# Kernel optimization log

Hardware: AMD Instinct MI355X
Metric: run time of the kernel (lower is better)

Reference implementation:

```python
import jax, jax.numpy as jnp
import numpy as np

WINDOW = 2


def _fo_pool(h, f):
    """c_t = f_t * c_{t-1} + (1 - f_t) * h_t with c_{-1} = 0, scanned over axis 1 (time).
    Implemented as an associative scan on affine maps (a, b): c -> a*c + b."""
    def combine(left, right):
        a1, b1 = left
        a2, b2 = right
        return a2 * a1, a2 * b1 + b2
    a = f
    b = (1.0 - f) * h
    _, c = jax.lax.associative_scan(combine, (a, b), axis=1)
    return c


def setup_inputs() -> dict:
    key = jax.random.key(0)
    k1, k2 = jax.random.split(key)
    B, T, C, U = 8, 2048, 1024, 1024
    x = jax.random.normal(k1, (B, T, C), dtype=jnp.float32)
    # Keras Conv1D kernel layout: [window, in_channels, out_channels]; glorot-ish scale
    scale = (2.0 / (C + 3 * U)) ** 0.5
    kernel = jax.random.normal(k2, (WINDOW, C, 3 * U), dtype=jnp.float32) * scale
    bias = jnp.zeros((3 * U,), dtype=jnp.float32)
    return {"x": x, "kernel": kernel, "bias": bias}


def reference(x, kernel, bias):
    # causal conv1d: pad (window-1) on the left of time axis
    gv = jax.lax.conv_general_dilated(
        x, kernel,
        window_strides=(1,),
        padding=[(WINDOW - 1, 0)],
        dimension_numbers=("NWC", "WIO", "NWC"),
    ) + bias  # [B, T, 3U]
    hidden, forget, output = jnp.split(gv, 3, axis=-1)
    hidden = jnp.tanh(hidden)
    forget = jax.nn.sigmoid(forget)
    c = _fo_pool(hidden, forget)           # [B, T, U]
    h = jax.nn.sigmoid(output) * c          # output gate
    return h
```

## Files before the change

### kernel.cpp

```cpp
#include <hip/hip_runtime.h>


typedef _Float16 f16;
typedef _Float16 f16x8 __attribute__((ext_vector_type(8)));
typedef float    f32x4 __attribute__((ext_vector_type(4)));

#define Bq 8
#define Tq 2048
#define Cq 1024
#define Uq 1024
#define Mq (Bq*Tq)
#define Kq (2*Cq)
#define Nq (3*Uq)
#define NCH 32
#define CHL (Tq/NCH)

#define AS1 __attribute__((address_space(1)))
#define AS3 __attribute__((address_space(3)))

__global__ void prep_xs(const float* __restrict__ x, f16* __restrict__ Xs) {
    long long idx = ((long long)blockIdx.x * blockDim.x + threadIdx.x) * 8;
    int c = (int)(idx & (Cq - 1));
    long long row = idx >> 10;
    int tp = (int)(row % (Tq + 1));
    int b  = (int)(row / (Tq + 1));
    f16x8 o;
    if (tp == 0) {
#pragma unroll
        for (int j = 0; j < 8; j++) o[j] = (f16)0.0f;
    } else {
        const float* src = x + (((size_t)b * Tq + (tp - 1)) << 10) + c;
        float4 v0 = *(const float4*)(src);
        float4 v1 = *(const float4*)(src + 4);
        o[0]=(f16)v0.x; o[1]=(f16)v0.y; o[2]=(f16)v0.z; o[3]=(f16)v0.w;
        o[4]=(f16)v1.x; o[5]=(f16)v1.y; o[6]=(f16)v1.z; o[7]=(f16)v1.w;
    }
    *(f16x8*)(Xs + idx) = o;
}

__global__ void prep_wt(const float* __restrict__ w, f16* __restrict__ WT) {
    __shared__ float t[32][33];
    int kb = blockIdx.x * 32, nb = blockIdx.y * 32;
    int tx = threadIdx.x & 31, ty = threadIdx.x >> 5;
#pragma unroll
    for (int j = 0; j < 32; j += 8)
        t[ty + j][tx] = w[(size_t)(kb + ty + j) * Nq + nb + tx];
    __syncthreads();
#pragma unroll
    for (int j = 0; j < 32; j += 8)
        WT[(size_t)(nb + ty + j) * Kq + kb + tx] = (f16)t[tx][ty + j];
}

__global__ __launch_bounds__(512, 2) void gemm_gates8(
    const f16* __restrict__ Xs, const f16* __restrict__ WT,
    const float* __restrict__ bias,
    f16* __restrict__ H, f16* __restrict__ F, f16* __restrict__ O)
{
    __shared__ __align__(16) f16 smem[65536];
    const int tid  = threadIdx.x;
    const int lane = tid & 63;
    const int wave = tid >> 6;
    const int wm = wave >> 2;
    const int wn = wave & 3;

    const int wg  = blockIdx.x;
    const int swz = (wg & 7) * 96 + (wg >> 3);
    const int mT  = swz / 12, nT = swz - mT * 12;
    const int rM  = mT * 256;
    const int nB  = nT * 256;
    const int b   = rM >> 11;
    const int t0  = rM & (Tq - 1);
    const size_t xsRow0 = (size_t)b * (Tq + 1) + t0;

    const int srow = tid >> 3;
    const int scol = (((tid & 7) ^ (srow & 7))) * 8;
    const f16* Abase = Xs + (xsRow0 + srow) * (size_t)Cq + scol;
    const f16* Bbase = WT + (size_t)(nB + srow) * Kq + scol;
    const int dstT = tid * 16;

#define STAGE_A(c, h, kt) do { \
    const f16* _s = Abase + (size_t)((h) * 128) * Cq + (kt) * 64; \
    int _d = (c) * 65536 + (h) * 16384 + dstT; \
    __builtin_amdgcn_global_load_lds((const AS1 void*)_s, \
        (AS3 void*)((char*)smem + _d), 16, 0, 0); \
    __builtin_amdgcn_global_load_lds((const AS1 void*)(_s + (size_t)64 * Cq), \
        (AS3 void*)((char*)smem + _d + 8192), 16, 0, 0); \
} while (0)

#define STAGE_B(c, h, kt) do { \
    const f16* _s = Bbase + (size_t)((h) * 128) * Kq + (kt) * 64; \
    int _d = 32768 + (c) * 65536 + (h) * 16384 + dstT; \
    __builtin_amdgcn_global_load_lds((const AS1 void*)_s, \
        (AS3 void*)((char*)smem + _d), 16, 0, 0); \
    __builtin_amdgcn_global_load_lds((const AS1 void*)(_s + (size_t)64 * Kq), \
        (AS3 void*)((char*)smem + _d + 8192), 16, 0, 0); \
} while (0)

    const int rAoff = (wm * 64 + (lane & 15)) * 128;
    const int rBoff = (wn * 32 + (lane & 15)) * 128;
    const int ksw0 = (((lane >> 4) * 16)) ^ ((lane & 7) << 4);
    const int ksw1 = (64 + ((lane >> 4) * 16)) ^ ((lane & 7) << 4);

    f32x4 acc[2][2][4][2] = {};
    f16x8 af[4][2], bg0[2][2], bg1[2][2];

#define LOADA(c, h) do { \
    const char* _a = (const char*)smem + (c) * 65536 + (h) * 16384 + rAoff; \
    _Pragma("unroll") \
    for (int mi = 0; mi < 4; mi++) { \
        af[mi][0] = *(const f16x8*)(_a + mi * 2048 + ksw0); \
        af[mi][1] = *(const f16x8*)(_a + mi * 2048 + ksw1); \
    } \
} while (0)

#define LOADB(c, g, breg) do { \
    const char* _b = (const char*)smem + 32768 + (c) * 65536 + (g) * 16384 + rBoff; \
    _Pragma("unroll") \
    for (int ni = 0; ni < 2; ni++) { \
        breg[ni][0] = *(const f16x8*)(_b + ni * 2048 + ksw0); \
        breg[ni][1] = *(const f16x8*)(_b + ni * 2048 + ksw1); \
    } \
} while (0)

#define MM(h, g, breg) do { \
    _Pragma("unroll") \
    for (int mi = 0; mi < 4; mi++) \
    _Pragma("unroll") \
    for (int ni = 0; ni < 2; ni++) { \
        acc[h][g][mi][ni] = __builtin_amdgcn_mfma_f32_16x16x32_f16(af[mi][0], breg[ni][0], acc[h][g][mi][ni], 0, 0, 0); \
        acc[h][g][mi][ni] = __builtin_amdgcn_mfma_f32_16x16x32_f16(af[mi][1], breg[ni][1], acc[h][g][mi][ni], 0, 0, 0); \
    } \
} while (0)

#define BAR() __builtin_amdgcn_s_barrier()
#define LGKM0() do { asm volatile("s_waitcnt lgkmcnt(0)" ::: "memory"); \
                     __builtin_amdgcn_sched_barrier(0); } while (0)
#define VM4() asm volatile("s_waitcnt vmcnt(4)" ::: "memory")

#define KTILE(c, ktn) do { \
     LOADA(c, 0); LOADB(c, 0, bg0); STAGE_A(1 - (c), 0, ktn); BAR(); LGKM0(); \
           __builtin_amdgcn_s_setprio(1); MM(0, 0, bg0); __builtin_amdgcn_s_setprio(0); VM4(); BAR(); \
     LOADB(c, 1, bg1); STAGE_B(1 - (c), 0, ktn); BAR(); LGKM0(); \
           __builtin_amdgcn_s_setprio(1); MM(0, 1, bg1); __builtin_amdgcn_s_setprio(0); VM4(); BAR(); \
     LOADA(c, 1); STAGE_B(1 - (c), 1, ktn); BAR(); LGKM0(); \
           __builtin_amdgcn_s_setprio(1); MM(1, 0, bg0); __builtin_amdgcn_s_setprio(0); BAR(); \
     STAGE_A(1 - (c), 1, ktn); BAR(); LGKM0(); \
           __builtin_amdgcn_s_setprio(1); MM(1, 1, bg1); __builtin_amdgcn_s_setprio(0); VM4(); BAR(); \
} while (0)

    STAGE_A(0, 0, 0); STAGE_B(0, 0, 0); STAGE_B(0, 1, 0); STAGE_A(0, 1, 0);
    asm volatile("s_waitcnt vmcnt(4)" ::: "memory");
    BAR();

    for (int t = 0; t < 32; t += 2) {
        KTILE(0, t + 1);
        KTILE(1, t + 2);
    }

    const int gate = nB >> 10;
    f16* G = (gate == 0) ? H : ((gate == 1) ? F : O);
#pragma unroll
    for (int h = 0; h < 2; h++)
#pragma unroll
    for (int g = 0; g < 2; g++)
#pragma unroll
    for (int ni = 0; ni < 2; ni++) {
        const int col = nB + g * 128 + wn * 32 + ni * 16 + (lane & 15);
        const int u = col & (Uq - 1);
        const float bv = bias[col];
#pragma unroll
        for (int mi = 0; mi < 4; mi++)
#pragma unroll
        for (int j = 0; j < 4; j++) {
            const int row = rM + h * 128 + wm * 64 + mi * 16 + ((lane >> 4) << 2) + j;
            float v = acc[h][g][mi][ni][j] + bv;
            float r;
            if (gate == 0) r = 1.0f - 2.0f / (__expf(2.0f * v) + 1.0f);
            else           r = 1.0f / (1.0f + __expf(-v));
            G[(size_t)row * Uq + u] = (f16)r;
        }
    }
}

__global__ void scan_pass1(const f16* __restrict__ F, const f16* __restrict__ H,
                           float* __restrict__ Ach, float* __restrict__ Bch) {
    int idx = blockIdx.x * blockDim.x + threadIdx.x;
    int u  = idx & (Uq - 1);
    int ch = (idx >> 10) & (NCH - 1);
    int b  = idx >> 15;
    size_t base = ((size_t)b * Tq + ch * CHL) * Uq + u;
    float a = 1.0f, c = 0.0f;
    for (int i = 0; i < CHL; i++) {
        float f = (float)F[base + (size_t)i * Uq];
        float h = (float)H[base + (size_t)i * Uq];
        c = f * c + (1.0f - f) * h;
        a *= f;
    }
    Ach[idx] = a;
    Bch[idx] = c;
}

__global__ void scan_pass2(const float* __restrict__ Ach, const float* __restrict__ Bch,
                           float* __restrict__ Cin) {
    int idx = blockIdx.x * blockDim.x + threadIdx.x;
    int u = idx & (Uq - 1);
    int b = idx >> 10;
    float c = 0.0f;
    for (int ch = 0; ch < NCH; ch++) {
        int o = ((b * NCH) + ch) * Uq + u;
        Cin[o] = c;
        c = Ach[o] * c + Bch[o];
    }
}

__global__ void scan_pass3(const f16* __restrict__ F, const f16* __restrict__ H,
                           const f16* __restrict__ O, const float* __restrict__ Cin,
                           float* __restrict__ out) {
    int idx = blockIdx.x * blockDim.x + threadIdx.x;
    int u  = idx & (Uq - 1);
    int ch = (idx >> 10) & (NCH - 1);
    int b  = idx >> 15;
    size_t base = ((size_t)b * Tq + ch * CHL) * Uq + u;
    float c = Cin[idx];
    for (int i = 0; i < CHL; i++) {
        float f = (float)F[base + (size_t)i * Uq];
        float h = (float)H[base + (size_t)i * Uq];
        c = f * c + (1.0f - f) * h;
        out[base + (size_t)i * Uq] = (float)O[base + (size_t)i * Uq] * c;
    }
}

extern "C" void kernel_launch(void* const* d_in, const int* in_sizes, int n_in,
                              void* d_out, int out_size, void* d_ws, size_t ws_size,
                              hipStream_t stream) {
    const float* x    = (const float*)d_in[0];
    const float* w    = (const float*)d_in[1];
    const float* bias = (const float*)d_in[2];
    float* out = (float*)d_out;
    char* ws = (char*)d_ws;

    f16* Xs   = (f16*)(ws);
    f16* WT   = (f16*)(ws + 33570816);
    f16* Hh   = (f16*)(ws + 46153728);
    f16* Fh   = (f16*)(ws + 79708160);
    f16* Oh   = (f16*)(ws + 113262592);
    float* Ach = (float*)(ws + 146817024);
    float* Bch = (float*)(ws + 147865600);
    float* Cin = (float*)(ws + 148914176);

    prep_xs<<<(Bq * (Tq + 1) * Cq) / (8 * 256), 256, 0, stream>>>(x, Xs);
    prep_wt<<<dim3(Kq / 32, Nq / 32), 256, 0, stream>>>(w, WT);
    gemm_gates8<<<(Mq / 256) * (Nq / 256), 512, 0, stream>>>(Xs, WT, bias, Hh, Fh, Oh);
    scan_pass1<<<(Bq * NCH * Uq) / 256, 256, 0, stream>>>(Fh, Hh, Ach, Bch);
    scan_pass2<<<(Bq * Uq) / 256, 256, 0, stream>>>(Ach, Bch, Cin);
    scan_pass3<<<(Bq * NCH * Uq) / 256, 256, 0, stream>>>(Fh, Hh, Oh, Cin, out);
}
```

Measured before the change: 261.8 us.

## Double-buffer A fragments and overlap LDS reads with MFMA using partial waitcnts

Splits the A register fragments into two buffers so the next fragment loads from LDS can be issued while MFMAs on the current fragments run. Full lgkmcnt(0) waits are replaced with partial lgkmcnt counts, several barriers are removed, and vmcnt waits are tightened from 4 to 2. The next tile's first A/B fragments are preloaded at the end of each k-tile. This raises register pressure and makes correctness depend on the chosen waitcnt counts and barrier placement.

```diff
diff --git a/kernel.cpp b/kernel.cpp
--- a/kernel.cpp
+++ b/kernel.cpp
@@ -102,18 +102,18 @@
     const int ksw1 = (64 + ((lane >> 4) * 16)) ^ ((lane & 7) << 4);
 
     f32x4 acc[2][2][4][2] = {};
-    f16x8 af[4][2], bg0[2][2], bg1[2][2];
-
-#define LOADA(c, h) do { \
+    f16x8 afA[4][2], afB[4][2], bg0[2][2], bg1[2][2];
+
+#define LOADA_TO(c, h, dst) do { \
     const char* _a = (const char*)smem + (c) * 65536 + (h) * 16384 + rAoff; \
     _Pragma("unroll") \
     for (int mi = 0; mi < 4; mi++) { \
-        af[mi][0] = *(const f16x8*)(_a + mi * 2048 + ksw0); \
-        af[mi][1] = *(const f16x8*)(_a + mi * 2048 + ksw1); \
+        dst[mi][0] = *(const f16x8*)(_a + mi * 2048 + ksw0); \
+        dst[mi][1] = *(const f16x8*)(_a + mi * 2048 + ksw1); \
     } \
 } while (0)
 
-#define LOADB(c, g, breg) do { \
+#define LOADB_TO(c, g, breg) do { \
     const char* _b = (const char*)smem + 32768 + (c) * 65536 + (g) * 16384 + rBoff; \
     _Pragma("unroll") \
     for (int ni = 0; ni < 2; ni++) { \
@@ -122,35 +122,45 @@
     } \
 } while (0)
 
-#define MM(h, g, breg) do { \
+#define MM(h, g, afr, breg) do { \
     _Pragma("unroll") \
     for (int mi = 0; mi < 4; mi++) \
     _Pragma("unroll") \
     for (int ni = 0; ni < 2; ni++) { \
-        acc[h][g][mi][ni] = __builtin_amdgcn_mfma_f32_16x16x32_f16(af[mi][0], breg[ni][0], acc[h][g][mi][ni], 0, 0, 0); \
-        acc[h][g][mi][ni] = __builtin_amdgcn_mfma_f32_16x16x32_f16(af[mi][1], breg[ni][1], acc[h][g][mi][ni], 0, 0, 0); \
+        acc[h][g][mi][ni] = __builtin_amdgcn_mfma_f32_16x16x32_f16(afr[mi][0], breg[ni][0], acc[h][g][mi][ni], 0, 0, 0); \
+        acc[h][g][mi][ni] = __builtin_amdgcn_mfma_f32_16x16x32_f16(afr[mi][1], breg[ni][1], acc[h][g][mi][ni], 0, 0, 0); \
     } \
 } while (0)
 
-#define BAR() __builtin_amdgcn_s_barrier()
-#define LGKM0() do { asm volatile("s_waitcnt lgkmcnt(0)" ::: "memory"); \
-                     __builtin_amdgcn_sched_barrier(0); } while (0)
-#define VM4() asm volatile("s_waitcnt vmcnt(4)" ::: "memory")
+#define BAR()  __builtin_amdgcn_s_barrier()
+#define SB0()  __builtin_amdgcn_sched_barrier(0)
+#define PRIO1  __builtin_amdgcn_s_setprio(1)
+#define PRIO0  __builtin_amdgcn_s_setprio(0)
+#define LGKMC(n) asm volatile("s_waitcnt lgkmcnt(" #n ")" ::: "memory")
+#define VM2()    asm volatile("s_waitcnt vmcnt(2)" ::: "memory")
 
 #define KTILE(c, ktn) do { \
-     LOADA(c, 0); LOADB(c, 0, bg0); STAGE_A(1 - (c), 0, ktn); BAR(); LGKM0(); \
-           __builtin_amdgcn_s_setprio(1); MM(0, 0, bg0); __builtin_amdgcn_s_setprio(0); VM4(); BAR(); \
-     LOADB(c, 1, bg1); STAGE_B(1 - (c), 0, ktn); BAR(); LGKM0(); \
-           __builtin_amdgcn_s_setprio(1); MM(0, 1, bg1); __builtin_amdgcn_s_setprio(0); VM4(); BAR(); \
-     LOADA(c, 1); STAGE_B(1 - (c), 1, ktn); BAR(); LGKM0(); \
-           __builtin_amdgcn_s_setprio(1); MM(1, 0, bg0); __builtin_amdgcn_s_setprio(0); BAR(); \
-     STAGE_A(1 - (c), 1, ktn); BAR(); LGKM0(); \
-           __builtin_amdgcn_s_setprio(1); MM(1, 1, bg1); __builtin_amdgcn_s_setprio(0); VM4(); BAR(); \
+     LOADB_TO(c, 1, bg1); STAGE_A(1 - (c), 0, ktn); \
+           SB0(); LGKMC(4); SB0(); \
+           PRIO1; MM(0, 0, afA, bg0); PRIO0; \
+           VM2(); BAR(); \
+     LOADA_TO(c, 1, afB); STAGE_B(1 - (c), 0, ktn); \
+           SB0(); LGKMC(8); SB0(); \
+           PRIO1; MM(0, 1, afA, bg1); PRIO0; \
+     STAGE_B(1 - (c), 1, ktn); \
+           SB0(); LGKMC(0); SB0(); \
+           PRIO1; MM(1, 0, afB, bg0); PRIO0; \
+           VM2(); BAR(); \
+     LOADA_TO(1 - (c), 0, afA); LOADB_TO(1 - (c), 0, bg0); STAGE_A(1 - (c), 1, ktn); \
+           SB0(); LGKMC(12); SB0(); \
+           PRIO1; MM(1, 1, afB, bg1); PRIO0; \
+           VM2(); BAR(); \
 } while (0)
 
     STAGE_A(0, 0, 0); STAGE_B(0, 0, 0); STAGE_B(0, 1, 0); STAGE_A(0, 1, 0);
-    asm volatile("s_waitcnt vmcnt(4)" ::: "memory");
+    asm volatile("s_waitcnt vmcnt(2)" ::: "memory");
     BAR();
+    LOADA_TO(0, 0, afA); LOADB_TO(0, 0, bg0);
 
     for (int t = 0; t < 32; t += 2) {
         KTILE(0, t + 1);
```

Measured after the change: 256.6 us. 2.0% less time.
